# Optimization experiments

Hardware: AMD Instinct MI355X
Metric: run time of the kernel (lower is better)

The kernel has to match this reference:

```python
import jax, jax.numpy as jnp
import numpy as np

IN_FEATURES = 512
OUT_FEATURES = 1024
ALPHA = 1.0
BATCH = 8192


def setup_inputs() -> dict:
    key = jax.random.key(0)
    kx, kw = jax.random.split(key)
    x = jax.random.normal(kx, (BATCH, IN_FEATURES), dtype=jnp.float32)
    # xavier_uniform for weight of shape (out, in): limit = sqrt(6/(fan_in+fan_out))
    limit = float(np.sqrt(6.0 / (IN_FEATURES + OUT_FEATURES)))
    weight = jax.random.uniform(kw, (OUT_FEATURES, IN_FEATURES), dtype=jnp.float32,
                                minval=-limit, maxval=limit)
    return {"x": x, "weight": weight}


def reference(x, weight):
    # dist: [B, K]
    x_sq = jnp.sum(x * x, axis=1, keepdims=True)            # [B, 1]
    w_sq = jnp.sum(weight * weight, axis=1)                  # [K]
    dist = x_sq + w_sq[None, :] - 2.0 * jnp.einsum('bd,kd->bk', x, weight)
    dist = jnp.maximum(dist, 0.0)
    # Student-t kernel soft assignment
    q = (1.0 + dist / ALPHA) ** (-(ALPHA + 1.0) / 2.0)       # [B, K]
    q = q / jnp.sum(q, axis=1, keepdims=True)                # row-normalize
    return q
```

## Files before the change

### kernel.cpp

```cpp
#include <hip/hip_runtime.h>
#include <hip/hip_bf16.h>

#define BATCH 8192
#define DIM   512
#define NCL   1024
#define ROWS  16
#define BK    32
#define NCH   (DIM / BK)
#define NWAVE 8

typedef __bf16 bf16x8 __attribute__((ext_vector_type(8)));
typedef float  f32x4  __attribute__((ext_vector_type(4)));

__device__ __forceinline__ unsigned short f2bf(float f) {
  union { float f; unsigned u; } v; v.f = f;
  unsigned r = v.u + 0x7fffu + ((v.u >> 16) & 1u);
  return (unsigned short)(r >> 16);
}
__device__ __forceinline__ unsigned pk(float a, float b) {
  return (unsigned)f2bf(a) | ((unsigned)f2bf(b) << 16);
}

__global__ __launch_bounds__(256) void prep_w(const float* __restrict__ w,
                                              __hip_bfloat16* __restrict__ wck,
                                              float* __restrict__ wsq) {
  int k    = blockIdx.x * 4 + (threadIdx.x >> 6);
  int lane = threadIdx.x & 63;
  const float4* wrow = (const float4*)(w + (size_t)k * DIM);
  float4 a = wrow[lane * 2 + 0];
  float4 b = wrow[lane * 2 + 1];
  float s = a.x*a.x + a.y*a.y + a.z*a.z + a.w*a.w
          + b.x*b.x + b.y*b.y + b.z*b.z + b.w*b.w;
  #pragma unroll
  for (int m = 32; m >= 1; m >>= 1) s += __shfl_xor(s, m, 64);
  if (lane == 0) wsq[k] = s;
  int c = lane >> 2;
  int j = (lane & 3) * 8;
  uint4 p = { pk(a.x, a.y), pk(a.z, a.w), pk(b.x, b.y), pk(b.z, b.w) };
  *(uint4*)(wck + ((size_t)c * NCL + k) * BK + j) = p;
}

__global__ __launch_bounds__(512, 4) void fused(const float* __restrict__ x,
                                                const __hip_bfloat16* __restrict__ wck,
                                                const float* __restrict__ wsq,
                                                float* __restrict__ out) {
  __shared__ __align__(16) __hip_bfloat16 xs2[NCH * 512];
  __shared__ float wsq_s[NCL];
  __shared__ float xsq_s[ROWS];
  __shared__ float red[ROWS][NWAVE + 1];
  __shared__ float rowtot[ROWS];

  const int tid = threadIdx.x;
  const int r0  = blockIdx.x * ROWS;

  const int wave = tid >> 6;
  const int lane = tid & 63;
  const int m16  = lane & 15;
  const int quad = lane >> 4;
  const int col0 = wave * 128;

  bf16x8 bcur[8];
  {
    const __hip_bfloat16* wp0 = wck + (size_t)(col0 + m16) * BK + quad * 8;
    #pragma unroll
    for (int ct = 0; ct < 8; ++ct)
      bcur[ct] = *(const bf16x8*)(wp0 + ct * (16 * BK));
  }

  {
    int row = tid >> 5;
    int seg = tid & 31;
    int c = seg >> 1, h = seg & 1;
    const f32x4* src = (const f32x4*)(x + (size_t)(r0 + row) * DIM + seg * 16);
    f32x4 v0 = src[0], v1 = src[1], v2 = src[2], v3 = src[3];
    float ss = v0.x*v0.x + v0.y*v0.y + v0.z*v0.z + v0.w*v0.w
             + v1.x*v1.x + v1.y*v1.y + v1.z*v1.z + v1.w*v1.w
             + v2.x*v2.x + v2.y*v2.y + v2.z*v2.z + v2.w*v2.w
             + v3.x*v3.x + v3.y*v3.y + v3.z*v3.z + v3.w*v3.w;
    __hip_bfloat16* base = xs2 + c * 512 + row * 8;
    uint4 p0 = { pk(v0.x, v0.y), pk(v0.z, v0.w), pk(v1.x, v1.y), pk(v1.z, v1.w) };
    uint4 p1 = { pk(v2.x, v2.y), pk(v2.z, v2.w), pk(v3.x, v3.y), pk(v3.z, v3.w) };
    *(uint4*)(base + (h * 2 + 0) * 128) = p0;
    *(uint4*)(base + (h * 2 + 1) * 128) = p1;
    ss += __shfl_xor(ss, 1, 64);
    ss += __shfl_xor(ss, 2, 64);
    ss += __shfl_xor(ss, 4, 64);
    ss += __shfl_xor(ss, 8, 64);
    ss += __shfl_xor(ss, 16, 64);
    if ((lane & 31) == 0) xsq_s[row] = ss;
    wsq_s[tid]       = wsq[tid];
    wsq_s[tid + 512] = wsq[tid + 512];
  }

  f32x4 acc[8];
  #pragma unroll
  for (int ct = 0; ct < 8; ++ct)
    acc[ct] = (f32x4){0.f, 0.f, 0.f, 0.f};

  __syncthreads();

  bf16x8 a_cur = *(const bf16x8*)(xs2 + lane * 8);

  #pragma unroll
  for (int c = 0; c < NCH; ++c) {
    bf16x8 bnx[8], a_nxt;
    if (c + 1 < NCH) {
      const __hip_bfloat16* wp = wck + ((size_t)(c + 1) * NCL + col0 + m16) * BK + quad * 8;
      #pragma unroll
      for (int ct = 0; ct < 8; ++ct)
        bnx[ct] = *(const bf16x8*)(wp + ct * (16 * BK));
      a_nxt = *(const bf16x8*)(xs2 + (c + 1) * 512 + lane * 8);
    }
    #pragma unroll
    for (int ct = 0; ct < 8; ++ct)
      acc[ct] = __builtin_amdgcn_mfma_f32_16x16x32_bf16(a_cur, bcur[ct], acc[ct], 0, 0, 0);
    if (c + 1 < NCH) {
      a_cur = a_nxt;
      #pragma unroll
      for (int ct = 0; ct < 8; ++ct) bcur[ct] = bnx[ct];
    }
  }

  float part[4] = {0.f, 0.f, 0.f, 0.f};
  float xq[4];
  #pragma unroll
  for (int i = 0; i < 4; ++i) xq[i] = xsq_s[quad * 4 + i];
  #pragma unroll
  for (int ct = 0; ct < 8; ++ct) {
    float wq = wsq_s[col0 + ct * 16 + m16];
    #pragma unroll
    for (int i = 0; i < 4; ++i) {
      float dist = fmaxf(xq[i] + wq - 2.f * acc[ct][i], 0.f);
      float qu = 1.f / (1.f + dist);
      acc[ct][i] = qu;
      part[i] += qu;
    }
  }
  #pragma unroll
  for (int i = 0; i < 4; ++i) {
    float s = part[i];
    s += __shfl_xor(s, 1, 64);
    s += __shfl_xor(s, 2, 64);
    s += __shfl_xor(s, 4, 64);
    s += __shfl_xor(s, 8, 64);
    part[i] = s;
  }
  if (m16 == 0) {
    #pragma unroll
    for (int i = 0; i < 4; ++i)
      red[quad * 4 + i][wave] = part[i];
  }
  __syncthreads();
  if (tid < ROWS) {
    float t = 0.f;
    #pragma unroll
    for (int w2 = 0; w2 < NWAVE; ++w2) t += red[tid][w2];
    rowtot[tid] = 1.f / t;
  }
  __syncthreads();
  #pragma unroll
  for (int i = 0; i < 4; ++i) {
    int r = quad * 4 + i;
    float inv = rowtot[r];
    float* orow = out + (size_t)(r0 + r) * NCL + col0 + m16;
    #pragma unroll
    for (int ct = 0; ct < 8; ++ct)
      orow[ct * 16] = acc[ct][i] * inv;
  }
}

extern "C" void kernel_launch(void* const* d_in, const int* in_sizes, int n_in,
                              void* d_out, int out_size, void* d_ws, size_t ws_size,
                              hipStream_t stream) {
  const float* x = (const float*)d_in[0];
  const float* w = (const float*)d_in[1];
  __hip_bfloat16* wck = (__hip_bfloat16*)d_ws;
  float* wsq = (float*)((char*)d_ws + (size_t)NCH * NCL * BK * 2);
  float* out = (float*)d_out;

  hipLaunchKernelGGL(prep_w, dim3(NCL / 4), dim3(256), 0, stream, w, wck, wsq);
  hipLaunchKernelGGL(fused, dim3(BATCH / ROWS), dim3(512), 0, stream, x, wck, wsq, out);
}
```

Measured before the change: 105.1 us.

## Process 32 rows per block with 16 waves and atomic row-sum reduction

Doubles the rows per block to 32 by using 1024 threads, two groups of 8 waves, each group computing 16 rows over all 1024 clusters. The x tile layout in shared memory gains a row-tile index. The two-step shared-memory row reduction is replaced by LDS atomicAdd into a per-row sum, removing one barrier. The grid is halved, which lowers per-block setup cost such as loading wsq into shared memory. Each weight chunk is still loaded separately by the wave in each row group, so global weight traffic is not reduced, and 1024-thread blocks may cut scheduling flexibility and occupancy.

After: 109.9 us. 1.05x slower.

```diff
diff --git a/kernel.cpp b/kernel.cpp
--- a/kernel.cpp
+++ b/kernel.cpp
@@ -4,10 +4,10 @@
 #define BATCH 8192
 #define DIM   512
 #define NCL   1024
-#define ROWS  16
+#define ROWS  32
 #define BK    32
 #define NCH   (DIM / BK)
-#define NWAVE 8
+#define NWAVE 16
 
 typedef __bf16 bf16x8 __attribute__((ext_vector_type(8)));
 typedef float  f32x4  __attribute__((ext_vector_type(4)));
@@ -40,15 +40,14 @@
   *(uint4*)(wck + ((size_t)c * NCL + k) * BK + j) = p;
 }
 
-__global__ __launch_bounds__(512, 4) void fused(const float* __restrict__ x,
-                                                const __hip_bfloat16* __restrict__ wck,
-                                                const float* __restrict__ wsq,
-                                                float* __restrict__ out) {
-  __shared__ __align__(16) __hip_bfloat16 xs2[NCH * 512];
+__global__ __launch_bounds__(1024, 4) void fused(const float* __restrict__ x,
+                                                 const __hip_bfloat16* __restrict__ wck,
+                                                 const float* __restrict__ wsq,
+                                                 float* __restrict__ out) {
+  __shared__ __align__(16) __hip_bfloat16 xs2[NCH * 2 * 512];
   __shared__ float wsq_s[NCL];
   __shared__ float xsq_s[ROWS];
-  __shared__ float red[ROWS][NWAVE + 1];
-  __shared__ float rowtot[ROWS];
+  __shared__ float rowsum[ROWS];
 
   const int tid = threadIdx.x;
   const int r0  = blockIdx.x * ROWS;
@@ -57,7 +56,8 @@
   const int lane = tid & 63;
   const int m16  = lane & 15;
   const int quad = lane >> 4;
-  const int col0 = wave * 128;
+  const int rt   = wave >> 3;
+  const int col0 = (wave & 7) * 128;
 
   bf16x8 bcur[8];
   {
@@ -71,13 +71,14 @@
     int row = tid >> 5;
     int seg = tid & 31;
     int c = seg >> 1, h = seg & 1;
+    int rw = row >> 4, m = row & 15;
     const f32x4* src = (const f32x4*)(x + (size_t)(r0 + row) * DIM + seg * 16);
     f32x4 v0 = src[0], v1 = src[1], v2 = src[2], v3 = src[3];
     float ss = v0.x*v0.x + v0.y*v0.y + v0.z*v0.z + v0.w*v0.w
              + v1.x*v1.x + v1.y*v1.y + v1.z*v1.z + v1.w*v1.w
              + v2.x*v2.x + v2.y*v2.y + v2.z*v2.z + v2.w*v2.w
              + v3.x*v3.x + v3.y*v3.y + v3.z*v3.z + v3.w*v3.w;
-    __hip_bfloat16* base = xs2 + c * 512 + row * 8;
+    __hip_bfloat16* base = xs2 + (c * 2 + rw) * 512 + m * 8;
     uint4 p0 = { pk(v0.x, v0.y), pk(v0.z, v0.w), pk(v1.x, v1.y), pk(v1.z, v1.w) };
     uint4 p1 = { pk(v2.x, v2.y), pk(v2.z, v2.w), pk(v3.x, v3.y), pk(v3.z, v3.w) };
     *(uint4*)(base + (h * 2 + 0) * 128) = p0;
@@ -88,8 +89,8 @@
     ss += __shfl_xor(ss, 8, 64);
     ss += __shfl_xor(ss, 16, 64);
     if ((lane & 31) == 0) xsq_s[row] = ss;
-    wsq_s[tid]       = wsq[tid];
-    wsq_s[tid + 512] = wsq[tid + 512];
+    wsq_s[tid] = wsq[tid];
+    if (tid < ROWS) rowsum[tid] = 0.f;
   }
 
   f32x4 acc[8];
@@ -99,7 +100,7 @@
 
   __syncthreads();
 
-  bf16x8 a_cur = *(const bf16x8*)(xs2 + lane * 8);
+  bf16x8 a_cur = *(const bf16x8*)(xs2 + (0 * 2 + rt) * 512 + lane * 8);
 
   #pragma unroll
   for (int c = 0; c < NCH; ++c) {
@@ -109,7 +110,7 @@
       #pragma unroll
       for (int ct = 0; ct < 8; ++ct)
         bnx[ct] = *(const bf16x8*)(wp + ct * (16 * BK));
-      a_nxt = *(const bf16x8*)(xs2 + (c + 1) * 512 + lane * 8);
+      a_nxt = *(const bf16x8*)(xs2 + ((c + 1) * 2 + rt) * 512 + lane * 8);
     }
     #pragma unroll
     for (int ct = 0; ct < 8; ++ct)
@@ -124,7 +125,7 @@
   float part[4] = {0.f, 0.f, 0.f, 0.f};
   float xq[4];
   #pragma unroll
-  for (int i = 0; i < 4; ++i) xq[i] = xsq_s[quad * 4 + i];
+  for (int i = 0; i < 4; ++i) xq[i] = xsq_s[rt * 16 + quad * 4 + i];
   #pragma unroll
   for (int ct = 0; ct < 8; ++ct) {
     float wq = wsq_s[col0 + ct * 16 + m16];
@@ -148,20 +149,13 @@
   if (m16 == 0) {
     #pragma unroll
     for (int i = 0; i < 4; ++i)
-      red[quad * 4 + i][wave] = part[i];
-  }
-  __syncthreads();
-  if (tid < ROWS) {
-    float t = 0.f;
-    #pragma unroll
-    for (int w2 = 0; w2 < NWAVE; ++w2) t += red[tid][w2];
-    rowtot[tid] = 1.f / t;
+      atomicAdd(&rowsum[rt * 16 + quad * 4 + i], part[i]);
   }
   __syncthreads();
   #pragma unroll
   for (int i = 0; i < 4; ++i) {
-    int r = quad * 4 + i;
-    float inv = rowtot[r];
+    int r = rt * 16 + quad * 4 + i;
+    float inv = 1.f / rowsum[r];
     float* orow = out + (size_t)(r0 + r) * NCL + col0 + m16;
     #pragma unroll
     for (int ct = 0; ct < 8; ++ct)
@@ -179,5 +173,5 @@
   float* out = (float*)d_out;
 
   hipLaunchKernelGGL(prep_w, dim3(NCL / 4), dim3(256), 0, stream, w, wck, wsq);
-  hipLaunchKernelGGL(fused, dim3(BATCH / ROWS), dim3(512), 0, stream, x, wck, wsq, out);
+  hipLaunchKernelGGL(fused, dim3(BATCH / ROWS), dim3(1024), 0, stream, x, wck, wsq, out);
 }
```
